# Kernel optimization log

Measured on AMD Instinct MI355X. Metric: run time of the kernel, lower is better.

## Reference

```python
import jax, jax.numpy as jnp
import numpy as np
from jax import lax

EPS = 1e-5
DW_THRESH = 4.0
PW_THRESH = 1e-3


def setup_inputs() -> dict:
    key = jax.random.key(0)
    ks = jax.random.split(key, 13)
    B, C, O, H, W = 32, 256, 256, 56, 56
    inp = {
        "x": jax.random.normal(ks[0], (B, C, H, W), jnp.float32),
        "dw_w": jax.random.normal(ks[1], (C, 1, 3, 3), jnp.float32) * 0.2,
        "dw_b": jax.random.normal(ks[2], (C,), jnp.float32) * 0.1,
        "bn1_gamma": 0.5 + jax.random.uniform(ks[3], (C,), jnp.float32) * 1.5,
        "bn1_beta": jax.random.normal(ks[4], (C,), jnp.float32) * 0.5,
        "bn1_mean": jax.random.normal(ks[5], (C,), jnp.float32) * 0.1,
        "bn1_var": 0.5 + jax.random.uniform(ks[6], (C,), jnp.float32),
        "pw_w": jax.random.normal(ks[7], (O, C, 1, 1), jnp.float32) * 0.06,
        "pw_b": jax.random.normal(ks[8], (O,), jnp.float32) * 0.1,
        "bn2_gamma": 0.5 + jax.random.uniform(ks[9], (O,), jnp.float32) * 1.5,
        "bn2_beta": jax.random.normal(ks[10], (O,), jnp.float32) * 0.5,
        "bn2_mean": jax.random.normal(ks[11], (O,), jnp.float32) * 0.1,
        "bn2_var": 0.5 + jax.random.uniform(ks[12], (O,), jnp.float32),
    }
    return inp


def _bn(x, gamma, beta, mean, var):
    # inference-mode BatchNorm2d over channel axis 1
    inv = gamma * lax.rsqrt(var + EPS)
    return x * inv[None, :, None, None] + (beta - mean * inv)[None, :, None, None]


def _cut(x, thresh):
    # per-(batch, channel) max-abs pruning: max(max(x), -min(x)) == max(|x|)
    max_abs = jnp.max(jnp.abs(x), axis=(2, 3))  # [B, C]
    return jnp.where((max_abs < thresh)[:, :, None, None], 0.0, x)


def reference(x, dw_w, dw_b, bn1_gamma, bn1_beta, bn1_mean, bn1_var,
              pw_w, pw_b, bn2_gamma, bn2_beta, bn2_mean, bn2_var):
    C = x.shape[1]
    # depthwise 3x3 conv, padding=1, groups=C
    y = lax.conv_general_dilated(
        x, dw_w, window_strides=(1, 1), padding=[(1, 1), (1, 1)],
        feature_group_count=C,
        dimension_numbers=("NCHW", "OIHW", "NCHW"),
    ) + dw_b[None, :, None, None]
    y = jax.nn.relu(_bn(y, bn1_gamma, bn1_beta, bn1_mean, bn1_var))
    y = _cut(y, DW_THRESH)
    # pointwise 1x1 conv as channel contraction
    z = jnp.einsum("bihw,oi->bohw", y, pw_w[:, :, 0, 0]) + pw_b[None, :, None, None]
    z = jax.nn.relu(_bn(z, bn2_gamma, bn2_beta, bn2_mean, bn2_var))
    z = _cut(z, PW_THRESH)
    return z
```

## Files before the change

### kernel.cpp

```cpp
#include <hip/hip_runtime.h>
#include <hip/hip_bf16.h>
#include <stdint.h>

#define BATCH 32
#define CIN   256
#define COUT  256
#define HW    3136
#define NPAD  3200

#define AS1 __attribute__((address_space(1)))
#define AS3 __attribute__((address_space(3)))

typedef short bf16x8 __attribute__((ext_vector_type(8)));
typedef float f32x4  __attribute__((ext_vector_type(4)));

__device__ __forceinline__ unsigned short f2bf(float f) {
    unsigned u = __float_as_uint(f);
    u += 0x7fffu + ((u >> 16) & 1u);
    return (unsigned short)(u >> 16);
}

__global__ __launch_bounds__(256) void prep_kernel(
        const float* __restrict__ pw_w, const float* __restrict__ pw_b,
        const float* __restrict__ g2, const float* __restrict__ be2,
        const float* __restrict__ mu2, const float* __restrict__ va2,
        unsigned short* __restrict__ Wp, float* __restrict__ b2,
        unsigned* __restrict__ pwmax) {
    int o = blockIdx.x;
    int t = threadIdx.x;
    float inv2 = g2[o] * rsqrtf(va2[o] + 1e-5f);
    Wp[o * CIN + t] = f2bf(pw_w[o * CIN + t] * inv2);
    if (t == 0) b2[o] = pw_b[o] * inv2 + be2[o] - mu2[o] * inv2;
    int idx = blockIdx.x * 256 + t;
    if (idx < BATCH * COUT) pwmax[idx] = 0u;
}

__global__ __launch_bounds__(256) void dw_kernel(
        const float* __restrict__ x, const float* __restrict__ dww,
        const float* __restrict__ dwb,
        const float* __restrict__ g1, const float* __restrict__ be1,
        const float* __restrict__ mu1, const float* __restrict__ va1,
        unsigned short* __restrict__ y, float* __restrict__ dwmax) {
    __shared__ float xs[4 * 3136];
    int tid  = threadIdx.x;
    int lane = tid & 63, wid = tid >> 6;
    int plane = blockIdx.x * 4 + wid;
    int c = plane & 255;

    const float* xp = x + (size_t)plane * HW;
    float* xw = xs + wid * 3136;

#pragma unroll
    for (int i = 0; i < 12; ++i)
        __builtin_amdgcn_global_load_lds(
            (const AS1 void*)(xp + i * 256 + lane * 4),
            (AS3 void*)(xw + i * 256), 16, 0, 0);
    __builtin_amdgcn_global_load_lds(
        (const AS1 void*)(xp + 3072 + lane),
        (AS3 void*)(xw + 3072), 4, 0, 0);

    float w00 = dww[c*9+0], w01 = dww[c*9+1], w02 = dww[c*9+2];
    float w10 = dww[c*9+3], w11 = dww[c*9+4], w12 = dww[c*9+5];
    float w20 = dww[c*9+6], w21 = dww[c*9+7], w22 = dww[c*9+8];
    float inv = g1[c] * rsqrtf(va1[c] + 1e-5f);
    float b0  = dwb[c] * inv + (be1[c] - mu1[c] * inv);

    int  col    = lane < 56 ? lane : 55;
    bool active = lane < 56;
    if (lane == 0)  { w00 = 0.f; w10 = 0.f; w20 = 0.f; }
    if (lane >= 55) { w02 = 0.f; w12 = 0.f; w22 = 0.f; }
    int il = (lane == 0) ? 0 : col - 1;
    int ir = (col == 55) ? 55 : col + 1;

    asm volatile("s_waitcnt vmcnt(0)" ::: "memory");
    __builtin_amdgcn_sched_barrier(0);

    const float* xb = xw;
    unsigned short* yp = y + (size_t)plane * NPAD + col;

    float A = 0.f;
    float Bv = 0.f;
    float lmax = 0.f;
#pragma unroll
    for (int q = 0; q < 56; q += 2) {
        float l0 = xb[q*56 + il],      c0 = xb[q*56 + col],      r0 = xb[q*56 + ir];
        float l1 = xb[(q+1)*56 + il],  c1 = xb[(q+1)*56 + col],  r1 = xb[(q+1)*56 + ir];
        if (q > 0) {
            float o0 = fmaf(l0, w20, fmaf(c0, w21, fmaf(r0, w22, A)));
            float v = fmaxf(fmaf(o0, inv, b0), 0.f);
            if (active) { lmax = fmaxf(lmax, v); yp[(q-1)*56] = f2bf(v); }
        }
        {
            float o1 = fmaf(l0, w10, fmaf(c0, w11, fmaf(r0, w12,
                       fmaf(l1, w20, fmaf(c1, w21, fmaf(r1, w22, Bv))))));
            float v = fmaxf(fmaf(o1, inv, b0), 0.f);
            if (active) { lmax = fmaxf(lmax, v); yp[q*56] = f2bf(v); }
        }
        float top0 = fmaf(l0, w00, fmaf(c0, w01, r0 * w02));
        A  = fmaf(l1, w10, fmaf(c1, w11, fmaf(r1, w12, top0)));
        Bv = fmaf(l1, w00, fmaf(c1, w01, r1 * w02));
    }
    {
        float v = fmaxf(fmaf(A, inv, b0), 0.f);
        if (active) { lmax = fmaxf(lmax, v); yp[55*56] = f2bf(v); }
    }
    for (int off = 32; off >= 1; off >>= 1)
        lmax = fmaxf(lmax, __shfl_xor(lmax, off, 64));
    if (lane == 0) dwmax[plane] = lmax;
    if (lane < 8) *(uint4*)(y + (size_t)plane * NPAD + HW + lane * 8)
        = make_uint4(0, 0, 0, 0);
}

__global__ __launch_bounds__(256, 2) void pw_kernel(
        const unsigned short* __restrict__ y, const unsigned short* __restrict__ Wp,
        const float* __restrict__ b2, const float* __restrict__ dwm,
        float* __restrict__ z, unsigned* __restrict__ pwmax) {
    __shared__ __align__(16) unsigned short Al[128 * 256];
    __shared__ __align__(16) unsigned short Bl[128 * 64];

    int bid0 = blockIdx.x;
    int bid = (bid0 & 7) * 200 + (bid0 >> 3);
    int mt = bid & 1;
    int rest = bid >> 1;
    int nt = rest % 25;
    int b = rest / 25;
    int m0 = mt * 128, n0 = nt * 128;

    int tid = threadIdx.x;
    int lane = tid & 63, wid = tid >> 6;
    int wm = (wid & 1) * 64, wn = (wid >> 1) * 64;
    int l15 = lane & 15, l4 = lane >> 4;

    const unsigned short* yb = y + (size_t)b * CIN * NPAD;
    const float* dwb_ = dwm + b * 256;

    const unsigned short* agsrc[4];
#pragma unroll
    for (int ii = 0; ii < 4; ++ii) {
        int s = ii * 256 + wid * 64 + lane;
        int m = s >> 3, cch = s & 7, dch = cch ^ (m & 7);
        agsrc[ii] = Wp + (size_t)(m0 + m) * CIN + dch * 8;
    }
    int bq[2], bnq[2];
    const unsigned short* bsrc[2];
#pragma unroll
    for (int i = 0; i < 2; ++i) {
        int u = tid + i * 256;
        bq[i] = u >> 5; bnq[i] = u & 31;
        bsrc[i] = yb + (size_t)(bq[i] * 4) * NPAD + n0 + bnq[i] * 4;
    }

#pragma unroll
    for (int ks = 0; ks < 4; ++ks)
#pragma unroll
        for (int ii = 0; ii < 4; ++ii)
            __builtin_amdgcn_global_load_lds(
                (const AS1 void*)(agsrc[ii] + ks * 64),
                (AS3 void*)((char*)Al + ks * 16384 + ii * 4096 + wid * 1024),
                16, 0, 0);
    __builtin_amdgcn_sched_barrier(0);

    uint2 breg[4][2][4];
    float4 fl[4][2];
#pragma unroll
    for (int kk = 0; kk < 4; ++kk) {
#pragma unroll
        for (int i = 0; i < 2; ++i)
#pragma unroll
            for (int r = 0; r < 4; ++r)
                breg[kk][i][r] = *(const uint2*)(bsrc[i] + (size_t)kk * 64 * NPAD + r * NPAD);
#pragma unroll
        for (int i = 0; i < 2; ++i)
            fl[kk][i] = *(const float4*)(dwb_ + kk * 64 + bq[i] * 4);
        __builtin_amdgcn_sched_barrier(0);
    }

    f32x4 acc[4][4];
#pragma unroll
    for (int mf = 0; mf < 4; ++mf)
#pragma unroll
        for (int nf = 0; nf < 4; ++nf) acc[mf][nf] = {0.f, 0.f, 0.f, 0.f};

#pragma unroll
    for (int kk = 0; kk < 4; ++kk) {
        if (kk == 0) asm volatile("s_waitcnt vmcnt(30)" ::: "memory");
        if (kk == 1) asm volatile("s_waitcnt vmcnt(20)" ::: "memory");
        if (kk == 2) asm volatile("s_waitcnt vmcnt(10)" ::: "memory");
        if (kk == 3) asm volatile("s_waitcnt vmcnt(0)"  ::: "memory");
        __builtin_amdgcn_sched_barrier(0);
#pragma unroll
        for (int i = 0; i < 2; ++i) {
            unsigned mk0 = fl[kk][i].x >= 4.0f ? 0xffffffffu : 0u;
            unsigned mk1 = fl[kk][i].y >= 4.0f ? 0xffffffffu : 0u;
            unsigned mk2 = fl[kk][i].z >= 4.0f ? 0xffffffffu : 0u;
            unsigned mk3 = fl[kk][i].w >= 4.0f ? 0xffffffffu : 0u;
            uint2 r0 = breg[kk][i][0], r1 = breg[kk][i][1];
            uint2 r2 = breg[kk][i][2], r3 = breg[kk][i][3];
            r0.x &= mk0; r0.y &= mk0; r1.x &= mk1; r1.y &= mk1;
            r2.x &= mk2; r2.y &= mk2; r3.x &= mk3; r3.y &= mk3;
            int q = bq[i], nq = bnq[i];
#pragma unroll
            for (int i2 = 0; i2 < 4; ++i2) {
                unsigned x0 = (i2 & 2) ? r0.y : r0.x;
                unsigned x1 = (i2 & 2) ? r1.y : r1.x;
                unsigned x2 = (i2 & 2) ? r2.y : r2.x;
                unsigned x3 = (i2 & 2) ? r3.y : r3.x;
                if (i2 & 1) { x0 >>= 16; x2 >>= 16; }
                else        { x0 &= 0xffffu; x2 &= 0xffffu; }
                unsigned px = (i2 & 1) ? (x0 | (x1 & 0xffff0000u))
                                       : (x0 | (x1 << 16));
                unsigned py = (i2 & 1) ? (x2 | (x3 & 0xffff0000u))
                                       : (x2 | (x3 << 16));
                int nloc = nq * 4 + i2;
                int sb = nloc * 128 + (((q >> 1) ^ ((nloc >> 2) & 7)) << 4) + ((q & 1) << 3);
                *(uint2*)((char*)Bl + sb) = make_uint2(px, py);
            }
        }
        asm volatile("s_waitcnt lgkmcnt(0)" ::: "memory");
        __builtin_amdgcn_s_barrier();
        __builtin_amdgcn_sched_barrier(0);
#pragma unroll
        for (int h = 0; h < 2; ++h) {
            bf16x8 af[4], bfr[4];
            int cc = h * 4 + l4;
#pragma unroll
            for (int mf = 0; mf < 4; ++mf) {
                int m = wm + mf * 16 + l15;
                af[mf] = *(const bf16x8*)((const char*)Al + kk * 16384
                             + m * 128 + ((cc ^ (m & 7)) << 4));
            }
#pragma unroll
            for (int nf = 0; nf < 4; ++nf) {
                int n = wn + nf * 16 + l15;
                bfr[nf] = *(const bf16x8*)((const char*)Bl + n * 128
                             + ((cc ^ ((n >> 2) & 7)) << 4));
            }
#pragma unroll
            for (int mf = 0; mf < 4; ++mf)
#pragma unroll
                for (int nf = 0; nf < 4; ++nf)
                    acc[mf][nf] = __builtin_amdgcn_mfma_f32_16x16x32_bf16(
                        af[mf], bfr[nf], acc[mf][nf], 0, 0, 0);
        }
        __builtin_amdgcn_s_barrier();
    }

    float* zb = z + (size_t)b * COUT * HW;
#pragma unroll
    for (int mf = 0; mf < 4; ++mf) {
        int obase = m0 + wm + mf * 16 + l4 * 4;
        float bb0 = b2[obase + 0], bb1 = b2[obase + 1];
        float bb2v = b2[obase + 2], bb3 = b2[obase + 3];
        float rmax[4] = {0.f, 0.f, 0.f, 0.f};
#pragma unroll
        for (int nf = 0; nf < 4; ++nf) {
            int n = n0 + wn + nf * 16 + l15;
            bool valid = (n < HW);
            float v0 = fmaxf(acc[mf][nf][0] + bb0, 0.f);
            float v1 = fmaxf(acc[mf][nf][1] + bb1, 0.f);
            float v2 = fmaxf(acc[mf][nf][2] + bb2v, 0.f);
            float v3 = fmaxf(acc[mf][nf][3] + bb3, 0.f);
            if (valid) {
                zb[(size_t)(obase + 0) * HW + n] = v0;
                zb[(size_t)(obase + 1) * HW + n] = v1;
                zb[(size_t)(obase + 2) * HW + n] = v2;
                zb[(size_t)(obase + 3) * HW + n] = v3;
                rmax[0] = fmaxf(rmax[0], v0);
                rmax[1] = fmaxf(rmax[1], v1);
                rmax[2] = fmaxf(rmax[2], v2);
                rmax[3] = fmaxf(rmax[3], v3);
            }
        }
#pragma unroll
        for (int r = 0; r < 4; ++r) {
            float v = rmax[r];
            v = fmaxf(v, __shfl_xor(v, 1, 64));
            v = fmaxf(v, __shfl_xor(v, 2, 64));
            v = fmaxf(v, __shfl_xor(v, 4, 64));
            v = fmaxf(v, __shfl_xor(v, 8, 64));
            if (l15 == 0)
                atomicMax(&pwmax[b * COUT + obase + r], __float_as_uint(v));
        }
    }
}

__global__ __launch_bounds__(256) void cut_kernel(const unsigned* __restrict__ pwmax,
                                                  float* __restrict__ z) {
    int base = blockIdx.x * 8;
#pragma unroll
    for (int j = 0; j < 8; ++j) {
        int bo = base + j;
        if (__uint_as_float(pwmax[bo]) >= 1e-3f) continue;
        float4* zp = (float4*)(z + (size_t)bo * HW);
        for (int i = threadIdx.x; i < HW / 4; i += 256)
            zp[i] = make_float4(0.f, 0.f, 0.f, 0.f);
    }
}

extern "C" void kernel_launch(void* const* d_in, const int* in_sizes, int n_in,
                              void* d_out, int out_size, void* d_ws, size_t ws_size,
                              hipStream_t stream) {
    const float* x   = (const float*)d_in[0];
    const float* dww = (const float*)d_in[1];
    const float* dwb = (const float*)d_in[2];
    const float* g1  = (const float*)d_in[3];
    const float* be1 = (const float*)d_in[4];
    const float* mu1 = (const float*)d_in[5];
    const float* va1 = (const float*)d_in[6];
    const float* pww = (const float*)d_in[7];
    const float* pwb = (const float*)d_in[8];
    const float* g2  = (const float*)d_in[9];
    const float* be2 = (const float*)d_in[10];
    const float* mu2 = (const float*)d_in[11];
    const float* va2 = (const float*)d_in[12];
    float* z = (float*)d_out;

    char* ws = (char*)d_ws;
    const size_t Y_BYTES = (size_t)BATCH * CIN * NPAD * 2;
    unsigned short* y  = (unsigned short*)ws;
    unsigned short* Wp = (unsigned short*)(ws + Y_BYTES);
    float* b2          = (float*)(ws + Y_BYTES + 131072);
    unsigned* pwmax    = (unsigned*)(ws + Y_BYTES + 131072 + 1024);
    float* dwmax       = (float*)(ws + Y_BYTES + 131072 + 1024 + 32768);

    prep_kernel<<<256, 256, 0, stream>>>(pww, pwb, g2, be2, mu2, va2, Wp, b2, pwmax);
    dw_kernel<<<2048, 256, 0, stream>>>(x, dww, dwb, g1, be1, mu1, va1, y, dwmax);
    pw_kernel<<<1600, 256, 0, stream>>>(y, Wp, b2, dwmax, z, pwmax);
    cut_kernel<<<BATCH * COUT / 8, 256, 0, stream>>>(pwmax, z);
}
```

Before: 100.8 us.

## Restructure pointwise GEMM into full-M 512-thread blocks with double-buffered B pipeline

The pointwise kernel now uses 512-thread blocks that cover all 256 output channels per N tile, so each y tile is read once instead of twice. It streams A slices through LDS per k-step and double-buffers the packed B tiles, overlapping global loads with MFMA work. The depthwise cut mask moves into dw_kernel, which zeroes pruned planes in y directly, removing the dwmax buffer and the masking in the GEMM. In exchange there are extra global stores for pruned planes, more barriers per k-step, and higher register and LDS pressure per block.

```diff
diff --git a/kernel.cpp b/kernel.cpp
--- a/kernel.cpp
+++ b/kernel.cpp
@@ -40,7 +40,7 @@
         const float* __restrict__ dwb,
         const float* __restrict__ g1, const float* __restrict__ be1,
         const float* __restrict__ mu1, const float* __restrict__ va1,
-        unsigned short* __restrict__ y, float* __restrict__ dwmax) {
+        unsigned short* __restrict__ y) {
     __shared__ float xs[4 * 3136];
     int tid  = threadIdx.x;
     int lane = tid & 63, wid = tid >> 6;
@@ -106,73 +106,120 @@
     }
     for (int off = 32; off >= 1; off >>= 1)
         lmax = fmaxf(lmax, __shfl_xor(lmax, off, 64));
-    if (lane == 0) dwmax[plane] = lmax;
     if (lane < 8) *(uint4*)(y + (size_t)plane * NPAD + HW + lane * 8)
         = make_uint4(0, 0, 0, 0);
-}
-
-__global__ __launch_bounds__(256, 2) void pw_kernel(
+    if (lmax < 4.0f) {
+        asm volatile("s_waitcnt vmcnt(0)" ::: "memory");
+        unsigned short* yp0 = y + (size_t)plane * NPAD;
+#pragma unroll
+        for (int it = 0; it < 7; ++it) {
+            int idx = it * 64 + lane;
+            if (idx < 392) *(uint4*)(yp0 + idx * 8) = make_uint4(0, 0, 0, 0);
+        }
+    }
+}
+
+__device__ __forceinline__ void load_raw(uint2* dst, const unsigned short* bsrc, int kk) {
+#pragma unroll
+    for (int r = 0; r < 4; ++r)
+        dst[r] = *(const uint2*)(bsrc + (size_t)(kk * 64 + r) * NPAD);
+}
+
+__device__ __forceinline__ void pack_b(const uint2* src, char* dstbase,
+                                       const int* sb_) {
+    uint2 r0 = src[0], r1 = src[1], r2 = src[2], r3 = src[3];
+#pragma unroll
+    for (int i2 = 0; i2 < 4; ++i2) {
+        unsigned x0 = (i2 & 2) ? r0.y : r0.x;
+        unsigned x1 = (i2 & 2) ? r1.y : r1.x;
+        unsigned x2 = (i2 & 2) ? r2.y : r2.x;
+        unsigned x3 = (i2 & 2) ? r3.y : r3.x;
+        if (i2 & 1) { x0 >>= 16; x2 >>= 16; }
+        else        { x0 &= 0xffffu; x2 &= 0xffffu; }
+        unsigned px = (i2 & 1) ? (x0 | (x1 & 0xffff0000u)) : (x0 | (x1 << 16));
+        unsigned py = (i2 & 1) ? (x2 | (x3 & 0xffff0000u)) : (x2 | (x3 << 16));
+        *(uint2*)(dstbase + sb_[i2]) = make_uint2(px, py);
+    }
+}
+
+__device__ __forceinline__ void read_af(bf16x8* af, const char* Al,
+                                        int wm, int l15, int l4) {
+#pragma unroll
+    for (int h = 0; h < 2; ++h)
+#pragma unroll
+        for (int mf = 0; mf < 4; ++mf) {
+            int m = wm + mf * 16 + l15;
+            int cc = h * 4 + l4;
+            af[h * 4 + mf] = *(const bf16x8*)(Al + m * 128 + ((cc ^ (m & 7)) << 4));
+        }
+}
+
+__device__ __forceinline__ void do_mfma(f32x4 (*acc)[4], const bf16x8* af,
+                                        const char* Blb, int wn, int l15, int l4) {
+#pragma unroll
+    for (int h = 0; h < 2; ++h) {
+        bf16x8 bfr[4];
+        int cc = h * 4 + l4;
+#pragma unroll
+        for (int nf = 0; nf < 4; ++nf) {
+            int n = wn + nf * 16 + l15;
+            bfr[nf] = *(const bf16x8*)(Blb + n * 128 + ((cc ^ ((n >> 2) & 7)) << 4));
+        }
+#pragma unroll
+        for (int mf = 0; mf < 4; ++mf)
+#pragma unroll
+            for (int nf = 0; nf < 4; ++nf)
+                acc[mf][nf] = __builtin_amdgcn_mfma_f32_16x16x32_bf16(
+                    af[h * 4 + mf], bfr[nf], acc[mf][nf], 0, 0, 0);
+    }
+}
+
+#define WAIT_V0_BAR  { asm volatile("s_waitcnt vmcnt(0)" ::: "memory");   \
+                       __builtin_amdgcn_sched_barrier(0);                  \
+                       __builtin_amdgcn_s_barrier();                       \
+                       __builtin_amdgcn_sched_barrier(0); }
+#define WAIT_LG_BAR  { asm volatile("s_waitcnt lgkmcnt(0)" ::: "memory"); \
+                       __builtin_amdgcn_sched_barrier(0);                  \
+                       __builtin_amdgcn_s_barrier();                       \
+                       __builtin_amdgcn_sched_barrier(0); }
+
+__global__ __launch_bounds__(512, 2) void pw_kernel(
         const unsigned short* __restrict__ y, const unsigned short* __restrict__ Wp,
-        const float* __restrict__ b2, const float* __restrict__ dwm,
-        float* __restrict__ z, unsigned* __restrict__ pwmax) {
-    __shared__ __align__(16) unsigned short Al[128 * 256];
-    __shared__ __align__(16) unsigned short Bl[128 * 64];
+        const float* __restrict__ b2, float* __restrict__ z,
+        unsigned* __restrict__ pwmax) {
+    __shared__ __align__(16) char lds[65536];
+    char* Al  = lds;
+    char* Bl0 = lds + 32768;
+    char* Bl1 = lds + 49152;
 
     int bid0 = blockIdx.x;
-    int bid = (bid0 & 7) * 200 + (bid0 >> 3);
-    int mt = bid & 1;
-    int rest = bid >> 1;
-    int nt = rest % 25;
-    int b = rest / 25;
-    int m0 = mt * 128, n0 = nt * 128;
+    int bid = (bid0 & 7) * 100 + (bid0 >> 3);
+    int b = bid / 25, nt = bid % 25;
+    int n0 = nt * 128;
 
     int tid = threadIdx.x;
     int lane = tid & 63, wid = tid >> 6;
-    int wm = (wid & 1) * 64, wn = (wid >> 1) * 64;
+    int wm = (wid >> 1) * 64, wn = (wid & 1) * 64;
     int l15 = lane & 15, l4 = lane >> 4;
 
     const unsigned short* yb = y + (size_t)b * CIN * NPAD;
-    const float* dwb_ = dwm + b * 256;
 
     const unsigned short* agsrc[4];
-#pragma unroll
-    for (int ii = 0; ii < 4; ++ii) {
-        int s = ii * 256 + wid * 64 + lane;
+    int aoff[4];
+#pragma unroll
+    for (int i = 0; i < 4; ++i) {
+        int s = i * 512 + tid;
         int m = s >> 3, cch = s & 7, dch = cch ^ (m & 7);
-        agsrc[ii] = Wp + (size_t)(m0 + m) * CIN + dch * 8;
-    }
-    int bq[2], bnq[2];
-    const unsigned short* bsrc[2];
-#pragma unroll
-    for (int i = 0; i < 2; ++i) {
-        int u = tid + i * 256;
-        bq[i] = u >> 5; bnq[i] = u & 31;
-        bsrc[i] = yb + (size_t)(bq[i] * 4) * NPAD + n0 + bnq[i] * 4;
-    }
-
-#pragma unroll
-    for (int ks = 0; ks < 4; ++ks)
-#pragma unroll
-        for (int ii = 0; ii < 4; ++ii)
-            __builtin_amdgcn_global_load_lds(
-                (const AS1 void*)(agsrc[ii] + ks * 64),
-                (AS3 void*)((char*)Al + ks * 16384 + ii * 4096 + wid * 1024),
-                16, 0, 0);
-    __builtin_amdgcn_sched_barrier(0);
-
-    uint2 breg[4][2][4];
-    float4 fl[4][2];
-#pragma unroll
-    for (int kk = 0; kk < 4; ++kk) {
-#pragma unroll
-        for (int i = 0; i < 2; ++i)
-#pragma unroll
-            for (int r = 0; r < 4; ++r)
-                breg[kk][i][r] = *(const uint2*)(bsrc[i] + (size_t)kk * 64 * NPAD + r * NPAD);
-#pragma unroll
-        for (int i = 0; i < 2; ++i)
-            fl[kk][i] = *(const float4*)(dwb_ + kk * 64 + bq[i] * 4);
-        __builtin_amdgcn_sched_barrier(0);
+        agsrc[i] = Wp + m * 256 + dch * 8;
+        aoff[i] = i * 8192 + wid * 1024;
+    }
+    int q = tid >> 5, nq = tid & 31;
+    const unsigned short* bsrc = yb + q * 4 * NPAD + n0 + nq * 4;
+    int sb_[4];
+#pragma unroll
+    for (int i2 = 0; i2 < 4; ++i2) {
+        int nloc = nq * 4 + i2;
+        sb_[i2] = nloc * 128 + (((q >> 1) ^ ((nloc >> 2) & 7)) << 4) + ((q & 1) << 3);
     }
 
     f32x4 acc[4][4];
@@ -181,74 +228,54 @@
 #pragma unroll
         for (int nf = 0; nf < 4; ++nf) acc[mf][nf] = {0.f, 0.f, 0.f, 0.f};
 
-#pragma unroll
-    for (int kk = 0; kk < 4; ++kk) {
-        if (kk == 0) asm volatile("s_waitcnt vmcnt(30)" ::: "memory");
-        if (kk == 1) asm volatile("s_waitcnt vmcnt(20)" ::: "memory");
-        if (kk == 2) asm volatile("s_waitcnt vmcnt(10)" ::: "memory");
-        if (kk == 3) asm volatile("s_waitcnt vmcnt(0)"  ::: "memory");
-        __builtin_amdgcn_sched_barrier(0);
-#pragma unroll
-        for (int i = 0; i < 2; ++i) {
-            unsigned mk0 = fl[kk][i].x >= 4.0f ? 0xffffffffu : 0u;
-            unsigned mk1 = fl[kk][i].y >= 4.0f ? 0xffffffffu : 0u;
-            unsigned mk2 = fl[kk][i].z >= 4.0f ? 0xffffffffu : 0u;
-            unsigned mk3 = fl[kk][i].w >= 4.0f ? 0xffffffffu : 0u;
-            uint2 r0 = breg[kk][i][0], r1 = breg[kk][i][1];
-            uint2 r2 = breg[kk][i][2], r3 = breg[kk][i][3];
-            r0.x &= mk0; r0.y &= mk0; r1.x &= mk1; r1.y &= mk1;
-            r2.x &= mk2; r2.y &= mk2; r3.x &= mk3; r3.y &= mk3;
-            int q = bq[i], nq = bnq[i];
-#pragma unroll
-            for (int i2 = 0; i2 < 4; ++i2) {
-                unsigned x0 = (i2 & 2) ? r0.y : r0.x;
-                unsigned x1 = (i2 & 2) ? r1.y : r1.x;
-                unsigned x2 = (i2 & 2) ? r2.y : r2.x;
-                unsigned x3 = (i2 & 2) ? r3.y : r3.x;
-                if (i2 & 1) { x0 >>= 16; x2 >>= 16; }
-                else        { x0 &= 0xffffu; x2 &= 0xffffu; }
-                unsigned px = (i2 & 1) ? (x0 | (x1 & 0xffff0000u))
-                                       : (x0 | (x1 << 16));
-                unsigned py = (i2 & 1) ? (x2 | (x3 & 0xffff0000u))
-                                       : (x2 | (x3 << 16));
-                int nloc = nq * 4 + i2;
-                int sb = nloc * 128 + (((q >> 1) ^ ((nloc >> 2) & 7)) << 4) + ((q & 1) << 3);
-                *(uint2*)((char*)Bl + sb) = make_uint2(px, py);
-            }
-        }
-        asm volatile("s_waitcnt lgkmcnt(0)" ::: "memory");
-        __builtin_amdgcn_s_barrier();
-        __builtin_amdgcn_sched_barrier(0);
-#pragma unroll
-        for (int h = 0; h < 2; ++h) {
-            bf16x8 af[4], bfr[4];
-            int cc = h * 4 + l4;
-#pragma unroll
-            for (int mf = 0; mf < 4; ++mf) {
-                int m = wm + mf * 16 + l15;
-                af[mf] = *(const bf16x8*)((const char*)Al + kk * 16384
-                             + m * 128 + ((cc ^ (m & 7)) << 4));
-            }
-#pragma unroll
-            for (int nf = 0; nf < 4; ++nf) {
-                int n = wn + nf * 16 + l15;
-                bfr[nf] = *(const bf16x8*)((const char*)Bl + n * 128
-                             + ((cc ^ ((n >> 2) & 7)) << 4));
-            }
-#pragma unroll
-            for (int mf = 0; mf < 4; ++mf)
-#pragma unroll
-                for (int nf = 0; nf < 4; ++nf)
-                    acc[mf][nf] = __builtin_amdgcn_mfma_f32_16x16x32_bf16(
-                        af[mf], bfr[nf], acc[mf][nf], 0, 0, 0);
-        }
-        __builtin_amdgcn_s_barrier();
-    }
+    uint2 rawA[4], rawB[4];
+    bf16x8 af[8];
+
+#define ISSUE_A(kk) {                                                        \
+    _Pragma("unroll")                                                        \
+    for (int i = 0; i < 4; ++i)                                              \
+        __builtin_amdgcn_global_load_lds(                                    \
+            (const AS1 void*)(agsrc[i] + (kk) * 64),                         \
+            (AS3 void*)(Al + aoff[i]), 16, 0, 0); }
+
+    ISSUE_A(0);
+    load_raw(rawA, bsrc, 0);
+    WAIT_V0_BAR;
+    pack_b(rawA, Bl0, sb_);
+    load_raw(rawB, bsrc, 1);
+    read_af(af, Al, wm, l15, l4);
+    WAIT_LG_BAR;
+    ISSUE_A(1);
+
+    do_mfma(acc, af, Bl0, wn, l15, l4);
+    WAIT_V0_BAR;
+    pack_b(rawB, Bl1, sb_);
+    load_raw(rawA, bsrc, 2);
+    read_af(af, Al, wm, l15, l4);
+    WAIT_LG_BAR;
+    ISSUE_A(2);
+
+    do_mfma(acc, af, Bl1, wn, l15, l4);
+    WAIT_V0_BAR;
+    pack_b(rawA, Bl0, sb_);
+    load_raw(rawB, bsrc, 3);
+    read_af(af, Al, wm, l15, l4);
+    WAIT_LG_BAR;
+    ISSUE_A(3);
+
+    do_mfma(acc, af, Bl0, wn, l15, l4);
+    WAIT_V0_BAR;
+    pack_b(rawB, Bl1, sb_);
+    read_af(af, Al, wm, l15, l4);
+    WAIT_LG_BAR;
+
+    do_mfma(acc, af, Bl1, wn, l15, l4);
+#undef ISSUE_A
 
     float* zb = z + (size_t)b * COUT * HW;
 #pragma unroll
     for (int mf = 0; mf < 4; ++mf) {
-        int obase = m0 + wm + mf * 16 + l4 * 4;
+        int obase = wm + mf * 16 + l4 * 4;
         float bb0 = b2[obase + 0], bb1 = b2[obase + 1];
         float bb2v = b2[obase + 2], bb3 = b2[obase + 3];
         float rmax[4] = {0.f, 0.f, 0.f, 0.f};
@@ -321,10 +348,9 @@
     unsigned short* Wp = (unsigned short*)(ws + Y_BYTES);
     float* b2          = (float*)(ws + Y_BYTES + 131072);
     unsigned* pwmax    = (unsigned*)(ws + Y_BYTES + 131072 + 1024);
-    float* dwmax       = (float*)(ws + Y_BYTES + 131072 + 1024 + 32768);
 
     prep_kernel<<<256, 256, 0, stream>>>(pww, pwb, g2, be2, mu2, va2, Wp, b2, pwmax);
-    dw_kernel<<<2048, 256, 0, stream>>>(x, dww, dwb, g1, be1, mu1, va1, y, dwmax);
-    pw_kernel<<<1600, 256, 0, stream>>>(y, Wp, b2, dwmax, z, pwmax);
+    dw_kernel<<<2048, 256, 0, stream>>>(x, dww, dwb, g1, be1, mu1, va1, y);
+    pw_kernel<<<800, 512, 0, stream>>>(y, Wp, b2, z, pwmax);
     cut_kernel<<<BATCH * COUT / 8, 256, 0, stream>>>(pwmax, z);
 }
```

New measurement: 101.9 us. About the same (+1.1%).

## Apply depthwise cut in dw kernel and retile pointwise GEMM to 64-row tiles

Applied to the files above, without the earlier changes.

The depthwise kernel now zeroes a whole y plane in place when its max is below the threshold, so the pointwise kernel no longer reads dwmax or applies masks. The pointwise kernel switches to 64-output-channel tiles with the full K of weights loaded into LDS once. Each wave packs its own B slice into private LDS, removing per-k block barriers, and B loads are software-pipelined one step ahead. The grid doubles and occupancy is raised to 3 blocks per CU, which lowers per-block MFMA reuse and means each y tile is read by four blocks instead of two.

```diff
diff --git a/kernel.cpp b/kernel.cpp
--- a/kernel.cpp
+++ b/kernel.cpp
@@ -40,7 +40,7 @@
         const float* __restrict__ dwb,
         const float* __restrict__ g1, const float* __restrict__ be1,
         const float* __restrict__ mu1, const float* __restrict__ va1,
-        unsigned short* __restrict__ y, float* __restrict__ dwmax) {
+        unsigned short* __restrict__ y) {
     __shared__ float xs[4 * 3136];
     int tid  = threadIdx.x;
     int lane = tid & 63, wid = tid >> 6;
@@ -106,154 +106,130 @@
     }
     for (int off = 32; off >= 1; off >>= 1)
         lmax = fmaxf(lmax, __shfl_xor(lmax, off, 64));
-    if (lane == 0) dwmax[plane] = lmax;
     if (lane < 8) *(uint4*)(y + (size_t)plane * NPAD + HW + lane * 8)
         = make_uint4(0, 0, 0, 0);
-}
-
-__global__ __launch_bounds__(256, 2) void pw_kernel(
+    if (lmax < 4.0f) {
+        asm volatile("s_waitcnt vmcnt(0)" ::: "memory");
+        unsigned short* yp0 = y + (size_t)plane * NPAD;
+#pragma unroll
+        for (int it = 0; it < 7; ++it) {
+            int idx = it * 64 + lane;
+            if (idx < 392) *(uint4*)(yp0 + idx * 8) = make_uint4(0, 0, 0, 0);
+        }
+    }
+}
+
+__global__ __launch_bounds__(256, 3) void pw_kernel(
         const unsigned short* __restrict__ y, const unsigned short* __restrict__ Wp,
-        const float* __restrict__ b2, const float* __restrict__ dwm,
-        float* __restrict__ z, unsigned* __restrict__ pwmax) {
-    __shared__ __align__(16) unsigned short Al[128 * 256];
-    __shared__ __align__(16) unsigned short Bl[128 * 64];
+        const float* __restrict__ b2, float* __restrict__ z,
+        unsigned* __restrict__ pwmax) {
+    __shared__ __align__(16) char lds[32768 + 16384];
+    char* Al = lds;
 
     int bid0 = blockIdx.x;
-    int bid = (bid0 & 7) * 200 + (bid0 >> 3);
-    int mt = bid & 1;
-    int rest = bid >> 1;
-    int nt = rest % 25;
-    int b = rest / 25;
-    int m0 = mt * 128, n0 = nt * 128;
-
-    int tid = threadIdx.x;
-    int lane = tid & 63, wid = tid >> 6;
-    int wm = (wid & 1) * 64, wn = (wid >> 1) * 64;
+    int bid  = (bid0 & 7) * 400 + (bid0 >> 3);
+    int nt   = bid % 25;
+    int rest = bid / 25;
+    int ot   = rest & 3;
+    int b    = rest >> 2;
+    int o0 = ot * 64, n0 = nt * 128;
+
+    int tid = threadIdx.x, lane = tid & 63, wid = tid >> 6;
+    char* Bw = lds + 32768 + wid * 4096;
+    int wn = wid * 32;
     int l15 = lane & 15, l4 = lane >> 4;
 
     const unsigned short* yb = y + (size_t)b * CIN * NPAD;
-    const float* dwb_ = dwm + b * 256;
-
-    const unsigned short* agsrc[4];
-#pragma unroll
-    for (int ii = 0; ii < 4; ++ii) {
-        int s = ii * 256 + wid * 64 + lane;
-        int m = s >> 3, cch = s & 7, dch = cch ^ (m & 7);
-        agsrc[ii] = Wp + (size_t)(m0 + m) * CIN + dch * 8;
-    }
-    int bq[2], bnq[2];
-    const unsigned short* bsrc[2];
-#pragma unroll
-    for (int i = 0; i < 2; ++i) {
-        int u = tid + i * 256;
-        bq[i] = u >> 5; bnq[i] = u & 31;
-        bsrc[i] = yb + (size_t)(bq[i] * 4) * NPAD + n0 + bnq[i] * 4;
-    }
-
-#pragma unroll
-    for (int ks = 0; ks < 4; ++ks)
-#pragma unroll
-        for (int ii = 0; ii < 4; ++ii)
-            __builtin_amdgcn_global_load_lds(
-                (const AS1 void*)(agsrc[ii] + ks * 64),
-                (AS3 void*)((char*)Al + ks * 16384 + ii * 4096 + wid * 1024),
-                16, 0, 0);
+
+#pragma unroll
+    for (int i = 0; i < 8; ++i) {
+        int s = i * 256 + tid;
+        int m = s >> 5, cch = s & 31, dch = cch ^ (m & 7);
+        __builtin_amdgcn_global_load_lds(
+            (const AS1 void*)(Wp + (size_t)(o0 + m) * CIN + dch * 8),
+            (AS3 void*)(Al + i * 4096 + wid * 1024), 16, 0, 0);
+    }
+
+    int l3 = lane & 7, q3 = lane >> 3;
+    const unsigned short* bbase = yb + n0 + wn + l3 * 4 + (size_t)(q3 * 4) * NPAD;
+
+    uint2 praw[2][4];
+#define LOADB(kk) { _Pragma("unroll") for (int i = 0; i < 2; ++i)             \
+                    _Pragma("unroll") for (int r = 0; r < 4; ++r)             \
+                      praw[i][r] = *(const uint2*)(bbase +                    \
+                          ((size_t)(kk) * 64 + i * 32 + r) * NPAD); }
+
+#define PACKB() { _Pragma("unroll") for (int i = 0; i < 2; ++i) {             \
+        int q = i * 8 + q3;                                                   \
+        uint2 r0 = praw[i][0], r1 = praw[i][1], r2 = praw[i][2], r3 = praw[i][3]; \
+        _Pragma("unroll") for (int i2 = 0; i2 < 4; ++i2) {                    \
+            unsigned x0 = (i2 & 2) ? r0.y : r0.x;                             \
+            unsigned x1 = (i2 & 2) ? r1.y : r1.x;                             \
+            unsigned x2 = (i2 & 2) ? r2.y : r2.x;                             \
+            unsigned x3 = (i2 & 2) ? r3.y : r3.x;                             \
+            if (i2 & 1) { x0 >>= 16; x2 >>= 16; }                             \
+            else        { x0 &= 0xffffu; x2 &= 0xffffu; }                     \
+            unsigned px = (i2 & 1) ? (x0 | (x1 & 0xffff0000u)) : (x0 | (x1 << 16)); \
+            unsigned py = (i2 & 1) ? (x2 | (x3 & 0xffff0000u)) : (x2 | (x3 << 16)); \
+            int nloc = l3 * 4 + i2;                                           \
+            int sb = nloc * 128 + (((q >> 1) ^ ((nloc >> 2) & 7)) << 4) + ((q & 1) << 3); \
+            *(uint2*)(Bw + sb) = make_uint2(px, py);                          \
+        } } }
+
+#define LGKM0 { asm volatile("s_waitcnt lgkmcnt(0)" ::: "memory");            \
+                __builtin_amdgcn_sched_barrier(0); }
+
+    f32x4 acc[4][2];
+#pragma unroll
+    for (int mf = 0; mf < 4; ++mf)
+#pragma unroll
+        for (int nf = 0; nf < 2; ++nf) acc[mf][nf] = {0.f, 0.f, 0.f, 0.f};
+
+#define STEP(kk) { _Pragma("unroll") for (int h = 0; h < 2; ++h) {            \
+        bf16x8 afr[4], bfr[2];                                                \
+        int cc = (kk) * 8 + h * 4 + l4;                                       \
+        _Pragma("unroll") for (int mf = 0; mf < 4; ++mf) {                    \
+            int m = mf * 16 + l15;                                            \
+            afr[mf] = *(const bf16x8*)(Al + m * 512 + ((cc ^ (m & 7)) << 4)); } \
+        int cb = h * 4 + l4;                                                  \
+        _Pragma("unroll") for (int nf = 0; nf < 2; ++nf) {                    \
+            int nloc = nf * 16 + l15;                                         \
+            bfr[nf] = *(const bf16x8*)(Bw + nloc * 128 + ((cb ^ ((nloc >> 2) & 7)) << 4)); } \
+        _Pragma("unroll") for (int mf = 0; mf < 4; ++mf)                      \
+            _Pragma("unroll") for (int nf = 0; nf < 2; ++nf)                  \
+                acc[mf][nf] = __builtin_amdgcn_mfma_f32_16x16x32_bf16(        \
+                    afr[mf], bfr[nf], acc[mf][nf], 0, 0, 0); } }
+
+    LOADB(0);
+    asm volatile("s_waitcnt vmcnt(8)" ::: "memory");
     __builtin_amdgcn_sched_barrier(0);
-
-    uint2 breg[4][2][4];
-    float4 fl[4][2];
-#pragma unroll
-    for (int kk = 0; kk < 4; ++kk) {
-#pragma unroll
-        for (int i = 0; i < 2; ++i)
-#pragma unroll
-            for (int r = 0; r < 4; ++r)
-                breg[kk][i][r] = *(const uint2*)(bsrc[i] + (size_t)kk * 64 * NPAD + r * NPAD);
-#pragma unroll
-        for (int i = 0; i < 2; ++i)
-            fl[kk][i] = *(const float4*)(dwb_ + kk * 64 + bq[i] * 4);
-        __builtin_amdgcn_sched_barrier(0);
-    }
-
-    f32x4 acc[4][4];
-#pragma unroll
-    for (int mf = 0; mf < 4; ++mf)
-#pragma unroll
-        for (int nf = 0; nf < 4; ++nf) acc[mf][nf] = {0.f, 0.f, 0.f, 0.f};
-
-#pragma unroll
-    for (int kk = 0; kk < 4; ++kk) {
-        if (kk == 0) asm volatile("s_waitcnt vmcnt(30)" ::: "memory");
-        if (kk == 1) asm volatile("s_waitcnt vmcnt(20)" ::: "memory");
-        if (kk == 2) asm volatile("s_waitcnt vmcnt(10)" ::: "memory");
-        if (kk == 3) asm volatile("s_waitcnt vmcnt(0)"  ::: "memory");
-        __builtin_amdgcn_sched_barrier(0);
-#pragma unroll
-        for (int i = 0; i < 2; ++i) {
-            unsigned mk0 = fl[kk][i].x >= 4.0f ? 0xffffffffu : 0u;
-            unsigned mk1 = fl[kk][i].y >= 4.0f ? 0xffffffffu : 0u;
-            unsigned mk2 = fl[kk][i].z >= 4.0f ? 0xffffffffu : 0u;
-            unsigned mk3 = fl[kk][i].w >= 4.0f ? 0xffffffffu : 0u;
-            uint2 r0 = breg[kk][i][0], r1 = breg[kk][i][1];
-            uint2 r2 = breg[kk][i][2], r3 = breg[kk][i][3];
-            r0.x &= mk0; r0.y &= mk0; r1.x &= mk1; r1.y &= mk1;
-            r2.x &= mk2; r2.y &= mk2; r3.x &= mk3; r3.y &= mk3;
-            int q = bq[i], nq = bnq[i];
-#pragma unroll
-            for (int i2 = 0; i2 < 4; ++i2) {
-                unsigned x0 = (i2 & 2) ? r0.y : r0.x;
-                unsigned x1 = (i2 & 2) ? r1.y : r1.x;
-                unsigned x2 = (i2 & 2) ? r2.y : r2.x;
-                unsigned x3 = (i2 & 2) ? r3.y : r3.x;
-                if (i2 & 1) { x0 >>= 16; x2 >>= 16; }
-                else        { x0 &= 0xffffu; x2 &= 0xffffu; }
-                unsigned px = (i2 & 1) ? (x0 | (x1 & 0xffff0000u))
-                                       : (x0 | (x1 << 16));
-                unsigned py = (i2 & 1) ? (x2 | (x3 & 0xffff0000u))
-                                       : (x2 | (x3 << 16));
-                int nloc = nq * 4 + i2;
-                int sb = nloc * 128 + (((q >> 1) ^ ((nloc >> 2) & 7)) << 4) + ((q & 1) << 3);
-                *(uint2*)((char*)Bl + sb) = make_uint2(px, py);
-            }
-        }
-        asm volatile("s_waitcnt lgkmcnt(0)" ::: "memory");
-        __builtin_amdgcn_s_barrier();
-        __builtin_amdgcn_sched_barrier(0);
-#pragma unroll
-        for (int h = 0; h < 2; ++h) {
-            bf16x8 af[4], bfr[4];
-            int cc = h * 4 + l4;
-#pragma unroll
-            for (int mf = 0; mf < 4; ++mf) {
-                int m = wm + mf * 16 + l15;
-                af[mf] = *(const bf16x8*)((const char*)Al + kk * 16384
-                             + m * 128 + ((cc ^ (m & 7)) << 4));
-            }
-#pragma unroll
-            for (int nf = 0; nf < 4; ++nf) {
-                int n = wn + nf * 16 + l15;
-                bfr[nf] = *(const bf16x8*)((const char*)Bl + n * 128
-                             + ((cc ^ ((n >> 2) & 7)) << 4));
-            }
-#pragma unroll
-            for (int mf = 0; mf < 4; ++mf)
-#pragma unroll
-                for (int nf = 0; nf < 4; ++nf)
-                    acc[mf][nf] = __builtin_amdgcn_mfma_f32_16x16x32_bf16(
-                        af[mf], bfr[nf], acc[mf][nf], 0, 0, 0);
-        }
-        __builtin_amdgcn_s_barrier();
-    }
+    __builtin_amdgcn_s_barrier();
+    __builtin_amdgcn_sched_barrier(0);
+    PACKB();
+    LGKM0;
+    LOADB(1);
+
+    STEP(0);
+    PACKB(); LGKM0; LOADB(2);
+    STEP(1);
+    PACKB(); LGKM0; LOADB(3);
+    STEP(2);
+    PACKB(); LGKM0;
+    STEP(3);
+
+#undef LOADB
+#undef PACKB
+#undef STEP
 
     float* zb = z + (size_t)b * COUT * HW;
 #pragma unroll
     for (int mf = 0; mf < 4; ++mf) {
-        int obase = m0 + wm + mf * 16 + l4 * 4;
+        int obase = o0 + mf * 16 + l4 * 4;
         float bb0 = b2[obase + 0], bb1 = b2[obase + 1];
         float bb2v = b2[obase + 2], bb3 = b2[obase + 3];
         float rmax[4] = {0.f, 0.f, 0.f, 0.f};
 #pragma unroll
-        for (int nf = 0; nf < 4; ++nf) {
+        for (int nf = 0; nf < 2; ++nf) {
             int n = n0 + wn + nf * 16 + l15;
             bool valid = (n < HW);
             float v0 = fmaxf(acc[mf][nf][0] + bb0, 0.f);
@@ -321,10 +297,9 @@
     unsigned short* Wp = (unsigned short*)(ws + Y_BYTES);
     float* b2          = (float*)(ws + Y_BYTES + 131072);
     unsigned* pwmax    = (unsigned*)(ws + Y_BYTES + 131072 + 1024);
-    float* dwmax       = (float*)(ws + Y_BYTES + 131072 + 1024 + 32768);
 
     prep_kernel<<<256, 256, 0, stream>>>(pww, pwb, g2, be2, mu2, va2, Wp, b2, pwmax);
-    dw_kernel<<<2048, 256, 0, stream>>>(x, dww, dwb, g1, be1, mu1, va1, y, dwmax);
-    pw_kernel<<<1600, 256, 0, stream>>>(y, Wp, b2, dwmax, z, pwmax);
+    dw_kernel<<<2048, 256, 0, stream>>>(x, dww, dwb, g1, be1, mu1, va1, y);
+    pw_kernel<<<3200, 256, 0, stream>>>(y, Wp, b2, z, pwmax);
     cut_kernel<<<BATCH * COUT / 8, 256, 0, stream>>>(pwmax, z);
 }
```

After: 121.5 us. 20.5% more time.
